# Optimization experiments

Measured on AMD Instinct MI355X. Metric: run time of the kernel, lower is better.

Reference implementation:

```python
import jax, jax.numpy as jnp
import numpy as np
from jax import lax

REG_STRENGTH = 0.01
TEMPERATURE = 0.1


def _pav_nonincreasing(y):
    """Pool-adjacent-violators for isotonic L2 regression with a
    nonincreasing constraint (matches torchsort's isotonic_l2).
    Returns (solution [n], block_id [n])."""
    n = y.shape[0]

    def body(carry, yi):
        m, c, t = carry  # block means, block counts, stack top
        m = m.at[t].set(yi)
        c = c.at[t].set(1)

        def cond(st):
            m_, c_, t_ = st
            return (t_ > 0) & (m_[t_ - 1] < m_[t_])

        def merge(st):
            m_, c_, t_ = st
            tot = m_[t_ - 1] * c_[t_ - 1] + m_[t_] * c_[t_]
            cc = c_[t_ - 1] + c_[t_]
            m_ = m_.at[t_ - 1].set(tot / cc)
            c_ = c_.at[t_ - 1].set(cc).at[t_].set(0)
            return (m_, c_, t_ - 1)

        m, c, t = lax.while_loop(cond, merge, (m, c, t))
        return (m, c, t + 1), None

    init = (jnp.zeros(n, y.dtype), jnp.zeros(n, jnp.int32), jnp.int32(0))
    (m, c, _), _ = lax.scan(body, init, y)
    sol = jnp.repeat(m, c, total_repeat_length=n)
    blk = jnp.repeat(jnp.arange(n), c, total_repeat_length=n)
    return sol, blk


@jax.custom_vjp
def _isotonic_l2(y):
    return _pav_nonincreasing(y)[0]


def _iso_fwd(y):
    sol, blk = _pav_nonincreasing(y)
    return sol, blk


def _iso_bwd(blk, g):
    n = g.shape[0]
    sums = jax.ops.segment_sum(g, blk, num_segments=n)
    cnts = jax.ops.segment_sum(jnp.ones_like(g), blk, num_segments=n)
    return ((sums / jnp.maximum(cnts, 1.0))[blk],)


_isotonic_l2.defvjp(_iso_fwd, _iso_bwd)


def soft_sort_ascending(scores, reg_strength):
    """torchsort.soft_sort with L2 regularization. scores: [B, R]."""
    n = scores.shape[-1]
    w = jnp.arange(n, 0, -1, dtype=scores.dtype) / reg_strength  # [n, ..., 1]/rs
    perm = jnp.argsort(scores, axis=-1)
    s = -jnp.take_along_axis(scores, perm, axis=-1)  # descending sort of -scores
    sol = jax.vmap(_isotonic_l2)(w[None, :] - s)
    return sol - w  # ascending soft-sorted values, [B, R]


def setup_inputs() -> dict:
    key = jax.random.key(0)
    k1, k2 = jax.random.split(key)
    scores = jax.random.normal(k1, (128, 8192), dtype=jnp.float32)
    ref_class = jax.random.randint(k2, (8192,), 0, 10, dtype=jnp.int32)
    return {"scores": scores, "ref_class": ref_class, "k": 32, "K": 8}


def reference(scores, ref_class, k, K):
    B, R = scores.shape
    rc = ref_class
    if rc.ndim == 1:
        rc = jnp.broadcast_to(rc[None, :], (B, R))
    rc = rc.astype(scores.dtype)
    sorted_vals = soft_sort_ascending(scores, REG_STRENGTH)  # [B, R]
    yk = sorted_vals[:, -k:]                                  # top-k largest, [B, k]
    M = jnp.abs(scores[:, None, :] - yk[:, :, None])          # [B, k, R]
    soft_mask = jax.nn.softmax(-M / TEMPERATURE, axis=-1)     # [B, k, R]
    soft_label_expectation = jnp.einsum('bkr,br->bk', soft_mask, rc)
    return yk, soft_label_expectation
```

## Files before the change

### kernel.cpp

```cpp
#include <hip/hip_runtime.h>
#include <math.h>

#define R_N    8192
#define K_TOP  32
#define CAND   1024
#define C1     14.426950408889634f
#define NEG_BIG (-3.0e38f)

__device__ __forceinline__ float fast_exp2(float x) {
#if __has_builtin(__builtin_amdgcn_exp2f)
    return __builtin_amdgcn_exp2f(x);
#else
    return exp2f(x);
#endif
}

__device__ __forceinline__ float merge_asc32(float v, int l) {
#pragma unroll
    for (int j = 16; j > 0; j >>= 1) {
        float pv = __shfl_xor(v, j, 64);
        v = ((l & j) == 0) ? fminf(v, pv) : fmaxf(v, pv);
    }
    return v;
}

__device__ __forceinline__ float sort32_asc(float v, int l) {
#pragma unroll
    for (int k = 2; k <= 32; k <<= 1) {
#pragma unroll
        for (int j = k >> 1; j > 0; j >>= 1) {
            float pv = __shfl_xor(v, j, 64);
            bool keep_min = (((l & k) == 0) == ((l & j) == 0));
            v = keep_min ? fminf(v, pv) : fmaxf(v, pv);
        }
    }
    return v;
}

__device__ __forceinline__ float sort64_asc(float v, int lane) {
#pragma unroll
    for (int k = 2; k <= 64; k <<= 1) {
#pragma unroll
        for (int j = k >> 1; j > 0; j >>= 1) {
            float pv = __shfl_xor(v, j, 64);
            bool keep_min = (((lane & k) == 0) == ((lane & j) == 0));
            v = keep_min ? fminf(v, pv) : fmaxf(v, pv);
        }
    }
    return v;
}

extern "C" __global__ void __launch_bounds__(1024)
k_fused(const float* __restrict__ scores, const int* __restrict__ rc,
        float* __restrict__ out, int B) {
    __shared__ float    cand[CAND];
    __shared__ float    topbuf[32 * 32];
    __shared__ float    twbuf[16];
    __shared__ float    yk_lds[K_TOP];
    __shared__ float    pbuf[16 * 2];
    __shared__ float    dsS[32], dsC[32];
    __shared__ unsigned cnt, dcnt;

    const int row  = blockIdx.x;
    const int tid  = threadIdx.x;
    const int lane = tid & 63;
    const int l    = tid & 31;
    const int h    = tid >> 5;
    const int wv   = tid >> 6;

    const float4* s4 = (const float4*)(scores + (size_t)row * R_N);
    const int4*   c4 = (const int4*)rc;
    float4 sa = s4[tid], sb = s4[tid + 1024];
    int4   ca = c4[tid], cb = c4[tid + 1024];
    float se[8] = {sa.x, sa.y, sa.z, sa.w, sb.x, sb.y, sb.z, sb.w};
    float ce[8] = {(float)ca.x, (float)ca.y, (float)ca.z, (float)ca.w,
                   (float)cb.x, (float)cb.y, (float)cb.z, (float)cb.w};

    cand[tid & (CAND - 1)] = NEG_BIG;
    if (tid == 0) { cnt = 0; dcnt = 0; }

    float tmax = se[0];
#pragma unroll
    for (int e = 1; e < 8; ++e) tmax = fmaxf(tmax, se[e]);
    float srt = sort64_asc(tmax, lane);
    float t_w = __shfl(srt, 32, 64);
    if (lane == 0) twbuf[wv] = t_w;
    __syncthreads();
    float t = twbuf[0];
#pragma unroll
    for (int w = 1; w < 16; ++w) t = fmaxf(t, twbuf[w]);

    unsigned long long m[8];
    unsigned tot = 0;
#pragma unroll
    for (int e = 0; e < 8; ++e) {
        m[e] = __ballot(se[e] >= t);
        tot += (unsigned)__popcll(m[e]);
    }
    unsigned wbase = 0;
    if (lane == 0) wbase = atomicAdd(&cnt, tot);
    wbase = __shfl(wbase, 0, 64);
    const unsigned long long ltm = (1ull << lane) - 1ull;
#pragma unroll
    for (int e = 0; e < 8; ++e) {
        if (se[e] >= t) {
            unsigned idx = wbase + (unsigned)__popcll(m[e] & ltm);
            if (idx < CAND) cand[idx] = se[e];
        }
        wbase += (unsigned)__popcll(m[e]);
    }
    __syncthreads();

    float run = sort32_asc(cand[tid], l);
#pragma unroll
    for (int stride = 1; stride < 32; stride <<= 1) {
        topbuf[h * 32 + l] = run;
        __syncthreads();
        if ((h & (2 * stride - 1)) == 0) {
            float pv = topbuf[(h + stride) * 32 + (l ^ 31)];
            run = merge_asc32(fmaxf(run, pv), l);
        }
        __syncthreads();
    }
    if (tid < 32) {
        yk_lds[l] = run;
        out[(size_t)row * K_TOP + l] = run;
    }
    __syncthreads();
    const float y0 = yk_lds[0];

    float P = 0.f, Pc = 0.f;
#pragma unroll
    for (int e = 0; e < 8; ++e) {
        if (se[e] <= y0) {
            float ex = fast_exp2(C1 * se[e]);
            P += ex;
            Pc = fmaf(ce[e], ex, Pc);
        } else {
            unsigned idx = atomicAdd(&dcnt, 1u);
            dsS[idx] = se[e];
            dsC[idx] = ce[e];
        }
    }
#pragma unroll
    for (int off = 32; off > 0; off >>= 1) {
        P  += __shfl_xor(P,  off, 64);
        Pc += __shfl_xor(Pc, off, 64);
    }
    if (lane == 0) { pbuf[wv * 2] = P; pbuf[wv * 2 + 1] = Pc; }
    __syncthreads();
    float Pt = 0.f, Pct = 0.f;
#pragma unroll
    for (int w = 0; w < 16; ++w) { Pt += pbuf[w * 2]; Pct += pbuf[w * 2 + 1]; }
    const int nD = (int)dcnt;

    const float yj0 = yk_lds[2 * wv];
    const float yj1 = yk_lds[2 * wv + 1];
    float n0 = 0.f, d0 = 0.f, n1 = 0.f, d1 = 0.f;
    if (lane < nD) {
        float s = dsS[lane], c = dsC[lane];
        float e0 = fast_exp2(-C1 * fabsf(s - yj0));
        float e1 = fast_exp2(-C1 * fabsf(s - yj1));
        d0 = e0; n0 = c * e0;
        d1 = e1; n1 = c * e1;
    }
#pragma unroll
    for (int off = 32; off > 0; off >>= 1) {
        n0 += __shfl_xor(n0, off, 64); d0 += __shfl_xor(d0, off, 64);
        n1 += __shfl_xor(n1, off, 64); d1 += __shfl_xor(d1, off, 64);
    }
    if (lane == 0) {
        float e0 = fast_exp2(-C1 * yj0);
        float e1 = fast_exp2(-C1 * yj1);
        float* dst = out + (size_t)B * K_TOP + (size_t)row * K_TOP + 2 * wv;
        dst[0] = fmaf(Pct, e0, n0) / fmaf(Pt, e0, d0);
        dst[1] = fmaf(Pct, e1, n1) / fmaf(Pt, e1, d1);
    }
}

extern "C" void kernel_launch(void* const* d_in, const int* in_sizes, int n_in,
                              void* d_out, int out_size, void* d_ws, size_t ws_size,
                              hipStream_t stream) {
    const float* scores = (const float*)d_in[0];
    const int*   rc     = (const int*)d_in[1];
    const int R = in_sizes[1];
    const int B = in_sizes[0] / R;
    float* out = (float*)d_out;

    hipLaunchKernelGGL(k_fused, dim3(B), dim3(1024), 0, stream, scores, rc, out, B);
}
```

Measured before the change: 66.00 us.

## Replace block-wide candidate tree with per-wave slabs and register merges

Each wavefront now uses its own 32nd-largest value as a local threshold and compacts its candidates into a private 128-entry LDS slab, so the shared atomic counter and the global threshold barrier are no longer needed. The final top-32 is built from per-wave bitonic sorts and in-register shuffle merges, which replaces the five-level LDS merge tree and its many __syncthreads. The exp2 of every score is computed early so it can overlap the sort, and the tail gives each half-wave one output so no work is duplicated. Per-wave thresholds let more candidates through, and slab overflow past 128 entries is dropped without detection. The slab is read back after only an lgkmcnt wait rather than a barrier, which relies on each wavefront reading only its own writes.

```diff
diff --git a/kernel.cpp b/kernel.cpp
--- a/kernel.cpp
+++ b/kernel.cpp
@@ -3,7 +3,7 @@
 
 #define R_N    8192
 #define K_TOP  32
-#define CAND   1024
+#define SLAB   128
 #define C1     14.426950408889634f
 #define NEG_BIG (-3.0e38f)
 
@@ -24,15 +24,11 @@
     return v;
 }
 
-__device__ __forceinline__ float sort32_asc(float v, int l) {
+__device__ __forceinline__ float merge_asc64(float v, int lane) {
 #pragma unroll
-    for (int k = 2; k <= 32; k <<= 1) {
-#pragma unroll
-        for (int j = k >> 1; j > 0; j >>= 1) {
-            float pv = __shfl_xor(v, j, 64);
-            bool keep_min = (((l & k) == 0) == ((l & j) == 0));
-            v = keep_min ? fminf(v, pv) : fmaxf(v, pv);
-        }
+    for (int j = 32; j > 0; j >>= 1) {
+        float pv = __shfl_xor(v, j, 64);
+        v = ((lane & j) == 0) ? fminf(v, pv) : fmaxf(v, pv);
     }
     return v;
 }
@@ -53,19 +49,17 @@
 extern "C" __global__ void __launch_bounds__(1024)
 k_fused(const float* __restrict__ scores, const int* __restrict__ rc,
         float* __restrict__ out, int B) {
-    __shared__ float    cand[CAND];
-    __shared__ float    topbuf[32 * 32];
-    __shared__ float    twbuf[16];
-    __shared__ float    yk_lds[K_TOP];
-    __shared__ float    pbuf[16 * 2];
+    __shared__ float    slab[16 * SLAB];
+    __shared__ float    lists[16 * 32];
     __shared__ float    dsS[32], dsC[32];
-    __shared__ unsigned cnt, dcnt;
+    __shared__ float    pbuf[32];
+    __shared__ unsigned dcnt;
 
     const int row  = blockIdx.x;
     const int tid  = threadIdx.x;
     const int lane = tid & 63;
-    const int l    = tid & 31;
-    const int h    = tid >> 5;
+    const int la   = tid & 31;
+    const int half = (tid >> 5) & 1;
     const int wv   = tid >> 6;
 
     const float4* s4 = (const float4*)(scores + (size_t)row * R_N);
@@ -76,66 +70,68 @@
     float ce[8] = {(float)ca.x, (float)ca.y, (float)ca.z, (float)ca.w,
                    (float)cb.x, (float)cb.y, (float)cb.z, (float)cb.w};
 
-    cand[tid & (CAND - 1)] = NEG_BIG;
-    if (tid == 0) { cnt = 0; dcnt = 0; }
+    if (tid == 0) dcnt = 0;
+
+    float ex[8];
+#pragma unroll
+    for (int e = 0; e < 8; ++e) ex[e] = fast_exp2(C1 * se[e]);
 
     float tmax = se[0];
 #pragma unroll
     for (int e = 1; e < 8; ++e) tmax = fmaxf(tmax, se[e]);
     float srt = sort64_asc(tmax, lane);
     float t_w = __shfl(srt, 32, 64);
-    if (lane == 0) twbuf[wv] = t_w;
-    __syncthreads();
-    float t = twbuf[0];
-#pragma unroll
-    for (int w = 1; w < 16; ++w) t = fmaxf(t, twbuf[w]);
 
-    unsigned long long m[8];
-    unsigned tot = 0;
+    slab[wv * SLAB + lane]      = NEG_BIG;
+    slab[wv * SLAB + 64 + lane] = NEG_BIG;
+    const unsigned long long ltm = (1ull << lane) - 1ull;
+    unsigned base = 0;
 #pragma unroll
     for (int e = 0; e < 8; ++e) {
-        m[e] = __ballot(se[e] >= t);
-        tot += (unsigned)__popcll(m[e]);
+        unsigned long long mm = __ballot(se[e] >= t_w);
+        if (se[e] >= t_w) {
+            unsigned idx = base + (unsigned)__popcll(mm & ltm);
+            if (idx < SLAB) slab[wv * SLAB + idx] = se[e];
+        }
+        base += (unsigned)__popcll(mm);
     }
-    unsigned wbase = 0;
-    if (lane == 0) wbase = atomicAdd(&cnt, tot);
-    wbase = __shfl(wbase, 0, 64);
-    const unsigned long long ltm = (1ull << lane) - 1ull;
-#pragma unroll
-    for (int e = 0; e < 8; ++e) {
-        if (se[e] >= t) {
-            unsigned idx = wbase + (unsigned)__popcll(m[e] & ltm);
-            if (idx < CAND) cand[idx] = se[e];
-        }
-        wbase += (unsigned)__popcll(m[e]);
-    }
+    __asm__ volatile("s_waitcnt lgkmcnt(0)" ::: "memory");
+
+    float r0 = slab[wv * SLAB + lane];
+    float r1 = slab[wv * SLAB + 64 + lane];
+    r0 = sort64_asc(r0, lane);
+    r1 = sort64_asc(r1, lane);
+    float hi = fmaxf(r0, __shfl_xor(r1, 63, 64));
+    hi = merge_asc64(hi, lane);
+    if (lane >= 32) lists[wv * 32 + (lane - 32)] = hi;
     __syncthreads();
 
-    float run = sort32_asc(cand[tid], l);
-#pragma unroll
-    for (int stride = 1; stride < 32; stride <<= 1) {
-        topbuf[h * 32 + l] = run;
-        __syncthreads();
-        if ((h & (2 * stride - 1)) == 0) {
-            float pv = topbuf[(h + stride) * 32 + (l ^ 31)];
-            run = merge_asc32(fmaxf(run, pv), l);
-        }
-        __syncthreads();
-    }
-    if (tid < 32) {
-        yk_lds[l] = run;
-        out[(size_t)row * K_TOP + l] = run;
-    }
-    __syncthreads();
-    const float y0 = yk_lds[0];
+    float v0 = lists[(8 * half + 0) * 32 + la];
+    float v1 = lists[(8 * half + 1) * 32 + la];
+    float v2 = lists[(8 * half + 2) * 32 + la];
+    float v3 = lists[(8 * half + 3) * 32 + la];
+    float v4 = lists[(8 * half + 4) * 32 + la];
+    float v5 = lists[(8 * half + 5) * 32 + la];
+    float v6 = lists[(8 * half + 6) * 32 + la];
+    float v7 = lists[(8 * half + 7) * 32 + la];
+    v0 = merge_asc32(fmaxf(v0, __shfl_xor(v1, 31, 64)), la);
+    v2 = merge_asc32(fmaxf(v2, __shfl_xor(v3, 31, 64)), la);
+    v4 = merge_asc32(fmaxf(v4, __shfl_xor(v5, 31, 64)), la);
+    v6 = merge_asc32(fmaxf(v6, __shfl_xor(v7, 31, 64)), la);
+    v0 = merge_asc32(fmaxf(v0, __shfl_xor(v2, 31, 64)), la);
+    v4 = merge_asc32(fmaxf(v4, __shfl_xor(v6, 31, 64)), la);
+    v0 = merge_asc32(fmaxf(v0, __shfl_xor(v4, 31, 64)), la);
+    float fin = merge_asc32(fmaxf(v0, __shfl_xor(v0, 63, 64)), la);
+
+    if (tid < 32) out[(size_t)row * K_TOP + tid] = fin;
+    const float y0 = __shfl(fin, 0, 64);
 
     float P = 0.f, Pc = 0.f;
 #pragma unroll
     for (int e = 0; e < 8; ++e) {
         if (se[e] <= y0) {
-            float ex = fast_exp2(C1 * se[e]);
-            P += ex;
-            Pc = fmaf(ce[e], ex, Pc);
+            P += ex[e];
+            Pc = fmaf(ce[e], ex[e], Pc);
         } else {
             unsigned idx = atomicAdd(&dcnt, 1u);
             dsS[idx] = se[e];
@@ -154,27 +150,24 @@
     for (int w = 0; w < 16; ++w) { Pt += pbuf[w * 2]; Pct += pbuf[w * 2 + 1]; }
     const int nD = (int)dcnt;
 
-    const float yj0 = yk_lds[2 * wv];
-    const float yj1 = yk_lds[2 * wv + 1];
-    float n0 = 0.f, d0 = 0.f, n1 = 0.f, d1 = 0.f;
-    if (lane < nD) {
-        float s = dsS[lane], c = dsC[lane];
-        float e0 = fast_exp2(-C1 * fabsf(s - yj0));
-        float e1 = fast_exp2(-C1 * fabsf(s - yj1));
-        d0 = e0; n0 = c * e0;
-        d1 = e1; n1 = c * e1;
+    const int   j  = 2 * wv + half;
+    const float yj = __shfl(fin, j, 64);
+    float d = 0.f, n = 0.f;
+    if (la < nD) {
+        float s = dsS[la], c = dsC[la];
+        float e_ = fast_exp2(-C1 * fabsf(s - yj));
+        d = e_;
+        n = c * e_;
     }
 #pragma unroll
-    for (int off = 32; off > 0; off >>= 1) {
-        n0 += __shfl_xor(n0, off, 64); d0 += __shfl_xor(d0, off, 64);
-        n1 += __shfl_xor(n1, off, 64); d1 += __shfl_xor(d1, off, 64);
+    for (int off = 16; off > 0; off >>= 1) {
+        d += __shfl_xor(d, off, 64);
+        n += __shfl_xor(n, off, 64);
     }
-    if (lane == 0) {
-        float e0 = fast_exp2(-C1 * yj0);
-        float e1 = fast_exp2(-C1 * yj1);
-        float* dst = out + (size_t)B * K_TOP + (size_t)row * K_TOP + 2 * wv;
-        dst[0] = fmaf(Pct, e0, n0) / fmaf(Pt, e0, d0);
-        dst[1] = fmaf(Pct, e1, n1) / fmaf(Pt, e1, d1);
+    if (la == 0) {
+        float e0 = fast_exp2(-C1 * yj);
+        out[(size_t)B * K_TOP + (size_t)row * K_TOP + j] =
+            fmaf(Pct, e0, n) / fmaf(Pt, e0, d);
     }
 }
 
```

New measurement: 68.32 us. 1.04x slower.
